# Performance work log

Measured on AMD Instinct MI355X. Metric: run time of the kernel, lower is better.

## Reference

```python
import jax, jax.numpy as jnp
import numpy as np

N = 50000      # nodes
E = 800000     # edges
IN = 128       # in_channels
HID = 128      # hidden_channels
R = 8          # num_relations
B = 4          # num_bases
EPS = 1e-5     # BatchNorm eps


def setup_inputs() -> dict:
    key = jax.random.key(0)
    ks = jax.random.split(key, 16)
    s = 0.05
    f = jnp.float32
    return {
        "x": jax.random.normal(ks[0], (N, IN), f),
        "edge_index": jax.random.randint(ks[1], (2, E), 0, N),
        "edge_type": jax.random.randint(ks[2], (E,), 0, R),
        # conv1 (RGCNConv with basis decomposition): W_r = sum_b comp[r,b] * bases[b]
        "comp1": jax.random.normal(ks[3], (R, B), f) * s,
        "bases1": jax.random.normal(ks[4], (B, IN, HID), f) * s,
        "root1": jax.random.normal(ks[5], (IN, HID), f) * s,
        "bias1": jnp.zeros((HID,), f),
        # skip1: Linear(in, hidden)
        "skip1_w": jax.random.normal(ks[6], (IN, HID), f) * s,
        "skip1_b": jnp.zeros((HID,), f),
        # BatchNorm(hidden)
        "bn_gamma": jnp.ones((HID,), f),
        "bn_beta": jnp.zeros((HID,), f),
        # conv2
        "comp2": jax.random.normal(ks[7], (R, B), f) * s,
        "bases2": jax.random.normal(ks[8], (B, HID, HID), f) * s,
        "root2": jax.random.normal(ks[9], (HID, HID), f) * s,
        "bias2": jnp.zeros((HID,), f),
        # skip2: Linear(hidden, hidden)
        "skip2_w": jax.random.normal(ks[10], (HID, HID), f) * s,
        "skip2_b": jnp.zeros((HID,), f),
    }


def rgcn_conv(x, src, dst, etype, comp, bases, root, bias):
    """PyG RGCNConv: per-relation mean aggregation + root weight + bias."""
    # Basis decomposition: W [R, d_in, d_out]
    W = jnp.einsum('rb,bdf->rdf', comp, bases)
    # Transform all nodes under every relation (node-level GEMM, avoids [E,B,F])
    h = jnp.einsum('nd,rdf->rnf', x, W)          # [R, N, F]
    msg = h[etype, src]                           # [E, F] gather per edge
    # mean per (dst, relation): normalize by relation-specific in-degree
    seg = dst * R + etype                         # combined segment id
    cnt = jax.ops.segment_sum(jnp.ones((msg.shape[0],), x.dtype), seg,
                              num_segments=N * R)
    msg = msg * (1.0 / jnp.maximum(cnt, 1.0))[seg][:, None]
    agg = jax.ops.segment_sum(msg, dst, num_segments=N)  # sum over relations
    return agg + x @ root + bias


def reference(x, edge_index, edge_type,
              comp1, bases1, root1, bias1, skip1_w, skip1_b,
              bn_gamma, bn_beta,
              comp2, bases2, root2, bias2, skip2_w, skip2_b):
    src, dst = edge_index[0], edge_index[1]
    # layer 1: conv + skip
    x1 = rgcn_conv(x, src, dst, edge_type, comp1, bases1, root1, bias1) \
         + x @ skip1_w + skip1_b
    h = x1  # captured pre-BatchNorm (i == num_layers - 1 branch)
    # BatchNorm (training-style batch stats) + ReLU; dropout = identity (eval)
    m = x1.mean(axis=0)
    v = x1.var(axis=0)
    xn = bn_gamma * (x1 - m) / jnp.sqrt(v + EPS) + bn_beta
    xr = jax.nn.relu(xn)
    # final layer: conv + skip
    x2 = rgcn_conv(xr, src, dst, edge_type, comp2, bases2, root2, bias2) \
         + xr @ skip2_w + skip2_b
    return (h, x2)
```

## Files before the change

### kernel.cpp

```cpp
#include <hip/hip_runtime.h>
#include <hip/hip_bf16.h>

#define Nn   50000
#define Ee   800000
#define RR   8
#define CAP  64
#define EPSV 1e-5f
#define NBLK 391
#define NSLICE 8
#define SLICE_N 6250

typedef unsigned int   u32;
typedef unsigned short u16;
typedef __attribute__((ext_vector_type(8))) short bf16x8;
typedef __attribute__((ext_vector_type(4))) float f32x4;

typedef __attribute__((address_space(1))) const void gvoid;
typedef __attribute__((address_space(3))) void lvoid;

__device__ __forceinline__ float bf2f(u16 u) {
    return __uint_as_float(((u32)u) << 16);
}
__device__ __forceinline__ u16 f2bf(float f) {
    u32 x = __float_as_uint(f);
    u32 r = (x + 0x7FFFu + ((x >> 16) & 1u)) >> 16;
    return (u16)r;
}
__device__ __forceinline__ u32 pack2(float a, float b) {
    return (u32)f2bf(a) | ((u32)f2bf(b) << 16);
}

__global__ void __launch_bounds__(256) setup(
        const float2* __restrict__ xf, u32* __restrict__ xb,
        const int* __restrict__ ei, const int* __restrict__ et,
        int* __restrict__ deg, int* __restrict__ buckets,
        const float* __restrict__ bases1, const float* __restrict__ root1,
        const float* __restrict__ skip1w, u16* __restrict__ wt1,
        const float* __restrict__ bases2, const float* __restrict__ root2,
        const float* __restrict__ skip2w, u16* __restrict__ wt2) {
    int b = blockIdx.x;
    if (b < 12500) {
        int t = b * 256 + threadIdx.x;
        float2 v = xf[t];
        xb[t] = pack2(v.x, v.y);
    } else if (b < 37500) {
        int bb = b - 12500;
        int slice = bb & 7;
        int e = (bb >> 3) * 256 + threadIdx.x;
        int dst = ei[Ee + e];
        if ((u32)(dst - slice * SLICE_N) < (u32)SLICE_N) {
            int src = ei[e];
            int rt  = et[e];
            int idx = atomicAdd(&deg[dst], 1);
            if (idx < CAP)
                buckets[dst * CAP + idx] = (src & 0xFFFF) | (rt << 16);
        }
    } else {
        const float *bs, *ro, *sk; u16* wt; int t;
        if (b < 37820) { t = (b - 37500) * 256 + threadIdx.x; bs = bases1; ro = root1; sk = skip1w; wt = wt1; }
        else           { t = (b - 37820) * 256 + threadIdx.x; bs = bases2; ro = root2; sk = skip2w; wt = wt2; }
        int c = t / 640, k = t % 640;
        float v;
        if (k < 512) {
            int bb = k >> 7, kk = k & 127;
            v = bs[(bb * 128 + kk) * 128 + c];
        } else {
            int kk = k - 512;
            v = ro[kk * 128 + c] + sk[kk * 128 + c];
        }
        wt[c * 640 + k] = f2bf(v);
    }
}

__global__ void __launch_bounds__(256, 8) aggregate(const u32* __restrict__ xrow,
                                                    const float* __restrict__ comp,
                                                    const int* __restrict__ deg,
                                                    const int* __restrict__ buckets,
                                                    u32* __restrict__ xcat) {
    __shared__ int   bk_s[4][CAP];
    __shared__ float scale_s[4][32];
    int wv = threadIdx.x >> 6, lane = threadIdx.x & 63;
    int node = blockIdx.x * 4 + wv;

    int d = deg[node];
    d = d < CAP ? d : CAP;
    const int* bk = buckets + node * CAP;

    int w0 = 0;
    if (lane < d) { w0 = bk[lane]; bk_s[wv][lane] = w0; }

    int rt0 = (lane < d) ? (w0 >> 16) : 8;
    int c[RR];
#pragma unroll
    for (int r = 0; r < RR; r++) c[r] = __popcll(__ballot(rt0 == r));

    if (lane < 32) {
        int cc = c[lane >> 2];
        scale_s[wv][lane] = comp[lane] / (float)(cc < 1 ? 1 : cc);
    }
    __syncthreads();

    float a0 = 0, a1 = 0, b0 = 0, b1 = 0, c0 = 0, c1 = 0, d0 = 0, d1 = 0;
    int i = 0;
    for (; i + 4 <= d; i += 4) {
        int e0 = bk_s[wv][i], e1 = bk_s[wv][i + 1];
        int e2 = bk_s[wv][i + 2], e3 = bk_s[wv][i + 3];
        u32 x0 = xrow[(e0 & 0xFFFF) * 64 + lane];
        u32 x1 = xrow[(e1 & 0xFFFF) * 64 + lane];
        u32 x2 = xrow[(e2 & 0xFFFF) * 64 + lane];
        u32 x3 = xrow[(e3 & 0xFFFF) * 64 + lane];
        f32x4 s0 = *(const f32x4*)&scale_s[wv][(e0 >> 16) * 4];
        f32x4 s1 = *(const f32x4*)&scale_s[wv][(e1 >> 16) * 4];
        f32x4 s2 = *(const f32x4*)&scale_s[wv][(e2 >> 16) * 4];
        f32x4 s3 = *(const f32x4*)&scale_s[wv][(e3 >> 16) * 4];
        float v0, v1;
        v0 = bf2f((u16)x0); v1 = bf2f((u16)(x0 >> 16));
        a0 += s0[0] * v0; a1 += s0[0] * v1; b0 += s0[1] * v0; b1 += s0[1] * v1;
        c0 += s0[2] * v0; c1 += s0[2] * v1; d0 += s0[3] * v0; d1 += s0[3] * v1;
        v0 = bf2f((u16)x1); v1 = bf2f((u16)(x1 >> 16));
        a0 += s1[0] * v0; a1 += s1[0] * v1; b0 += s1[1] * v0; b1 += s1[1] * v1;
        c0 += s1[2] * v0; c1 += s1[2] * v1; d0 += s1[3] * v0; d1 += s1[3] * v1;
        v0 = bf2f((u16)x2); v1 = bf2f((u16)(x2 >> 16));
        a0 += s2[0] * v0; a1 += s2[0] * v1; b0 += s2[1] * v0; b1 += s2[1] * v1;
        c0 += s2[2] * v0; c1 += s2[2] * v1; d0 += s2[3] * v0; d1 += s2[3] * v1;
        v0 = bf2f((u16)x3); v1 = bf2f((u16)(x3 >> 16));
        a0 += s3[0] * v0; a1 += s3[0] * v1; b0 += s3[1] * v0; b1 += s3[1] * v1;
        c0 += s3[2] * v0; c1 += s3[2] * v1; d0 += s3[3] * v0; d1 += s3[3] * v1;
    }
    for (; i < d; i++) {
        int ee = bk_s[wv][i];
        u32 xv = xrow[(ee & 0xFFFF) * 64 + lane];
        f32x4 ss = *(const f32x4*)&scale_s[wv][(ee >> 16) * 4];
        float v0 = bf2f((u16)xv), v1 = bf2f((u16)(xv >> 16));
        a0 += ss[0] * v0; a1 += ss[0] * v1; b0 += ss[1] * v0; b1 += ss[1] * v1;
        c0 += ss[2] * v0; c1 += ss[2] * v1; d0 += ss[3] * v0; d1 += ss[3] * v1;
    }

    u32* orow = xcat + node * 256;
    orow[0 * 64 + lane] = pack2(a0, a1);
    orow[1 * 64 + lane] = pack2(b0, b1);
    orow[2 * 64 + lane] = pack2(c0, c1);
    orow[3 * 64 + lane] = pack2(d0, d1);
}

__global__ void __launch_bounds__(256, 1) gemm_x(const u16* __restrict__ xcat,
                                                 const u16* __restrict__ xrow,
                                                 const u16* __restrict__ wt,
                                                 const float* __restrict__ biasA,
                                                 const float* __restrict__ biasB,
                                                 float* __restrict__ out,
                                                 float* __restrict__ bnsum,
                                                 int do_stats) {
    int t = threadIdx.x, w = t >> 6, lane = t & 63;
    int lm = lane & 15, hk = lane >> 4;
    int mw = (blockIdx.x * 4 + w) * 32;

    int r0 = mw + lm;      r0 = r0 < Nn ? r0 : Nn - 1;
    int r1 = mw + 16 + lm; r1 = r1 < Nn ? r1 : Nn - 1;
    const u16* a0p = xcat + r0 * 512 + hk * 8;
    const u16* a1p = xcat + r1 * 512 + hk * 8;
    const u16* x0p = xrow + r0 * 128 + hk * 8;
    const u16* x1p = xrow + r1 * 128 + hk * 8;
    const u16* bp  = wt + lm * 640 + hk * 8;

    f32x4 acc[2][8];
#pragma unroll
    for (int fr = 0; fr < 2; fr++)
#pragma unroll
        for (int g = 0; g < 8; g++) acc[fr][g] = (f32x4){0, 0, 0, 0};

#pragma unroll
    for (int it = 0; it < 10; it++) {
#pragma unroll
        for (int ks = 0; ks < 2; ks++) {
            int ko = it * 64 + ks * 32;
            bf16x8 a0, a1;
            if (it < 8) {
                a0 = *(const bf16x8*)(a0p + ko);
                a1 = *(const bf16x8*)(a1p + ko);
            } else {
                int kx = (it - 8) * 64 + ks * 32;
                a0 = *(const bf16x8*)(x0p + kx);
                a1 = *(const bf16x8*)(x1p + kx);
            }
#pragma unroll
            for (int g = 0; g < 8; g++) {
                bf16x8 b = *(const bf16x8*)(bp + g * 10240 + ko);
                acc[0][g] = __builtin_amdgcn_mfma_f32_16x16x32_bf16(a0, b, acc[0][g], 0, 0, 0);
                acc[1][g] = __builtin_amdgcn_mfma_f32_16x16x32_bf16(a1, b, acc[1][g], 0, 0, 0);
            }
        }
    }

    float lsum[8], lsq[8];
#pragma unroll
    for (int g = 0; g < 8; g++) { lsum[g] = 0.f; lsq[g] = 0.f; }
#pragma unroll
    for (int fr = 0; fr < 2; fr++)
#pragma unroll
        for (int g = 0; g < 8; g++) {
            int cc = g * 16 + lm;
            float bias = biasA[cc] + biasB[cc];
#pragma unroll
            for (int i = 0; i < 4; i++) {
                int grow = mw + fr * 16 + hk * 4 + i;
                if (grow < Nn) {
                    float v = acc[fr][g][i] + bias;
                    out[grow * 128 + cc] = v;
                    lsum[g] += v; lsq[g] += v * v;
                }
            }
        }
    if (do_stats) {
#pragma unroll
        for (int g = 0; g < 8; g++) {
            lsum[g] += __shfl_xor(lsum[g], 16); lsum[g] += __shfl_xor(lsum[g], 32);
            lsq[g]  += __shfl_xor(lsq[g], 16);  lsq[g]  += __shfl_xor(lsq[g], 32);
        }
        if (hk == 0) {
#pragma unroll
            for (int g = 0; g < 8; g++) {
                int cc = g * 16 + lm;
                atomicAdd(&bnsum[cc], lsum[g]);
                atomicAdd(&bnsum[128 + cc], lsq[g]);
            }
        }
    }
}

__global__ void __launch_bounds__(256) bn_relu(const float2* __restrict__ h,
                                               const float* __restrict__ bnsum,
                                               const float* __restrict__ gamma,
                                               const float* __restrict__ beta,
                                               u32* __restrict__ xr) {
    __shared__ float ab_s[256];
    int tid = threadIdx.x;
    if (tid < 128) {
        float m   = bnsum[tid] * (1.0f / Nn);
        float ex2 = bnsum[128 + tid] * (1.0f / Nn);
        float var = ex2 - m * m;
        float s   = gamma[tid] * rsqrtf(var + EPSV);
        ab_s[tid]       = s;
        ab_s[128 + tid] = beta[tid] - m * s;
    }
    __syncthreads();
    int t = blockIdx.x * 256 + tid;
    int c0 = (tid & 63) * 2;
    float2 hv = h[t];
    float v0 = hv.x * ab_s[c0] + ab_s[128 + c0];
    float v1 = hv.y * ab_s[c0 + 1] + ab_s[128 + c0 + 1];
    v0 = v0 > 0.f ? v0 : 0.f;
    v1 = v1 > 0.f ? v1 : 0.f;
    xr[t] = pack2(v0, v1);
}

extern "C" void kernel_launch(void* const* d_in, const int* in_sizes, int n_in,
                              void* d_out, int out_size, void* d_ws, size_t ws_size,
                              hipStream_t stream) {
    const float* x      = (const float*)d_in[0];
    const int*   ei     = (const int*)d_in[1];
    const int*   et     = (const int*)d_in[2];
    const float* comp1  = (const float*)d_in[3];
    const float* bases1 = (const float*)d_in[4];
    const float* root1  = (const float*)d_in[5];
    const float* bias1  = (const float*)d_in[6];
    const float* skip1w = (const float*)d_in[7];
    const float* skip1b = (const float*)d_in[8];
    const float* gamma  = (const float*)d_in[9];
    const float* beta   = (const float*)d_in[10];
    const float* comp2  = (const float*)d_in[11];
    const float* bases2 = (const float*)d_in[12];
    const float* root2  = (const float*)d_in[13];
    const float* bias2  = (const float*)d_in[14];
    const float* skip2w = (const float*)d_in[15];
    const float* skip2b = (const float*)d_in[16];
    float* out = (float*)d_out;

    char* ws = (char*)d_ws;
    int*   deg     = (int*)(ws + 0);
    float* bnsum   = (float*)(ws + 200000);
    int*   buckets = (int*)(ws + 202240);
    u16*   wt1     = (u16*)(ws + 13002240);
    u16*   wt2     = (u16*)(ws + 13166080);
    u32*   xb      = (u32*)(ws + 13329920);
    u32*   xr      = xb;
    u16*   xcat    = (u16*)(ws + 26129920);

    hipMemsetAsync(deg, 0, 201024, stream);

    setup<<<38140, 256, 0, stream>>>((const float2*)x, xb, ei, et, deg, buckets,
                                     bases1, root1, skip1w, wt1,
                                     bases2, root2, skip2w, wt2);

    aggregate<<<Nn / 4, 256, 0, stream>>>(xb, comp1, deg, buckets, (u32*)xcat);
    gemm_x<<<NBLK, 256, 0, stream>>>(xcat, (const u16*)xb, wt1, bias1, skip1b,
                                     out, bnsum, 1);

    bn_relu<<<Nn / 4, 256, 0, stream>>>((const float2*)out, bnsum, gamma, beta, xr);

    aggregate<<<Nn / 4, 256, 0, stream>>>(xr, comp2, deg, buckets, (u32*)xcat);
    gemm_x<<<NBLK, 256, 0, stream>>>(xcat, (const u16*)xr, wt2, bias2, skip2b,
                                     out + Nn * 128, bnsum, 0);
}
```

Baseline: 364.0 us.

## Stage GEMM A/B tiles in LDS via direct global-to-LDS loads with swizzle

The node GEMM previously had each wave read its A rows and the full weight matrix B straight from global memory into registers. Now each 128-row block cooperatively copies 128x64 tiles of A and B into XOR-swizzled shared memory using global_load_lds, then feeds MFMA from LDS. This lets the four waves share the B tile and cuts redundant global traffic. The cost is two barriers per K step with no double buffering, so load and compute do not overlap. The launch bound also drops the one-block-per-CU minimum, which may allow higher occupancy.

```diff
diff --git a/kernel.cpp b/kernel.cpp
--- a/kernel.cpp
+++ b/kernel.cpp
@@ -17,6 +17,10 @@
 
 typedef __attribute__((address_space(1))) const void gvoid;
 typedef __attribute__((address_space(3))) void lvoid;
+
+__device__ __forceinline__ void gl_lds16(const void* g, void* l) {
+    __builtin_amdgcn_global_load_lds((gvoid*)g, (lvoid*)l, 16, 0, 0);
+}
 
 __device__ __forceinline__ float bf2f(u16 u) {
     return __uint_as_float(((u32)u) << 16);
@@ -143,53 +147,69 @@
     orow[3 * 64 + lane] = pack2(d0, d1);
 }
 
-__global__ void __launch_bounds__(256, 1) gemm_x(const u16* __restrict__ xcat,
-                                                 const u16* __restrict__ xrow,
-                                                 const u16* __restrict__ wt,
-                                                 const float* __restrict__ biasA,
-                                                 const float* __restrict__ biasB,
-                                                 float* __restrict__ out,
-                                                 float* __restrict__ bnsum,
-                                                 int do_stats) {
+__global__ void __launch_bounds__(256) gemm_x(const u16* __restrict__ xcat,
+                                              const u16* __restrict__ xrow,
+                                              const u16* __restrict__ wt,
+                                              const float* __restrict__ biasA,
+                                              const float* __restrict__ biasB,
+                                              float* __restrict__ out,
+                                              float* __restrict__ bnsum,
+                                              int do_stats) {
+    __shared__ u16 As[128 * 64];
+    __shared__ u16 Bs[128 * 64];
+
     int t = threadIdx.x, w = t >> 6, lane = t & 63;
+    int m0 = blockIdx.x * 128;
     int lm = lane & 15, hk = lane >> 4;
-    int mw = (blockIdx.x * 4 + w) * 32;
-
-    int r0 = mw + lm;      r0 = r0 < Nn ? r0 : Nn - 1;
-    int r1 = mw + 16 + lm; r1 = r1 < Nn ? r1 : Nn - 1;
-    const u16* a0p = xcat + r0 * 512 + hk * 8;
-    const u16* a1p = xcat + r1 * 512 + hk * 8;
-    const u16* x0p = xrow + r0 * 128 + hk * 8;
-    const u16* x1p = xrow + r1 * 128 + hk * 8;
-    const u16* bp  = wt + lm * 640 + hk * 8;
-
+
+    const u16* agp[4]; const u16* axp[4]; char* alp[4];
+    const u16* bgp[4]; char* blp[4];
+#pragma unroll
+    for (int j = 0; j < 4; j++) {
+        int f = j * 256 + t;
+        int row = f >> 3, kc = (f & 7) ^ (row & 7);
+        int gr = m0 + row; gr = gr < Nn ? gr : Nn - 1;
+        agp[j] = xcat + gr * 512 + kc * 8;
+        axp[j] = xrow + gr * 128 + kc * 8;
+        alp[j] = (char*)As + j * 4096 + w * 1024;
+        bgp[j] = wt + row * 640 + kc * 8;
+        blp[j] = (char*)Bs + j * 4096 + w * 1024;
+    }
+
+    int wr = w * 32;
     f32x4 acc[2][8];
 #pragma unroll
     for (int fr = 0; fr < 2; fr++)
 #pragma unroll
         for (int g = 0; g < 8; g++) acc[fr][g] = (f32x4){0, 0, 0, 0};
 
-#pragma unroll
     for (int it = 0; it < 10; it++) {
+        if (it < 8) {
+            int ko = it * 64;
+#pragma unroll
+            for (int j = 0; j < 4; j++) gl_lds16(agp[j] + ko, alp[j]);
+        } else {
+            int ko = (it - 8) * 64;
+#pragma unroll
+            for (int j = 0; j < 4; j++) gl_lds16(axp[j] + ko, alp[j]);
+        }
+        int kb = it * 64;
+#pragma unroll
+        for (int j = 0; j < 4; j++) gl_lds16(bgp[j] + kb, blp[j]);
+        __syncthreads();
 #pragma unroll
         for (int ks = 0; ks < 2; ks++) {
-            int ko = it * 64 + ks * 32;
-            bf16x8 a0, a1;
-            if (it < 8) {
-                a0 = *(const bf16x8*)(a0p + ko);
-                a1 = *(const bf16x8*)(a1p + ko);
-            } else {
-                int kx = (it - 8) * 64 + ks * 32;
-                a0 = *(const bf16x8*)(x0p + kx);
-                a1 = *(const bf16x8*)(x1p + kx);
-            }
+            int sw = (((ks * 4 + hk) ^ (lm & 7)) * 16);
+            bf16x8 a0 = *(const bf16x8*)((const char*)As + (wr + lm) * 128 + sw);
+            bf16x8 a1 = *(const bf16x8*)((const char*)As + (wr + 16 + lm) * 128 + sw);
 #pragma unroll
             for (int g = 0; g < 8; g++) {
-                bf16x8 b = *(const bf16x8*)(bp + g * 10240 + ko);
+                bf16x8 b = *(const bf16x8*)((const char*)Bs + (g * 16 + lm) * 128 + sw);
                 acc[0][g] = __builtin_amdgcn_mfma_f32_16x16x32_bf16(a0, b, acc[0][g], 0, 0, 0);
                 acc[1][g] = __builtin_amdgcn_mfma_f32_16x16x32_bf16(a1, b, acc[1][g], 0, 0, 0);
             }
         }
+        __syncthreads();
     }
 
     float lsum[8], lsq[8];
@@ -203,7 +223,7 @@
             float bias = biasA[cc] + biasB[cc];
 #pragma unroll
             for (int i = 0; i < 4; i++) {
-                int grow = mw + fr * 16 + hk * 4 + i;
+                int grow = m0 + wr + fr * 16 + hk * 4 + i;
                 if (grow < Nn) {
                     float v = acc[fr][g][i] + bias;
                     out[grow * 128 + cc] = v;
```

New measurement: 309.8 us. -14.9%, faster.
